# Kernel optimization log

Hardware: AMD Instinct MI355X
Metric: run time of the kernel (lower is better)

Reference implementation:

```python
import jax, jax.numpy as jnp
import numpy as np

B, D, K = 4, 128, 512   # batch, node_embedding_dim, num_nodes
ALPHA = 0.2             # LeakyReLU negative slope


def setup_inputs() -> dict:
    key = jax.random.key(0)
    k1, k2, k3, k4 = jax.random.split(key, 4)
    x = jax.random.normal(k1, (B, D, K), dtype=jnp.float32)
    # nn.Linear(2D -> D): store weight as (2D, D) for right-multiplication
    lin_w = jax.random.normal(k2, (2 * D, D), dtype=jnp.float32) * (1.0 / np.sqrt(2 * D))
    lin_b = jax.random.normal(k3, (D,), dtype=jnp.float32) * 0.01
    # attention vector a: (D,) (xavier-uniform in torch; scale-equivalent normal here)
    a = jax.random.normal(k4, (D,), dtype=jnp.float32) * (1.414 * np.sqrt(2.0 / (D + 1)))
    bias_mat = jnp.zeros((K, K), dtype=jnp.float32)  # init zeros per module
    return {"x": x, "lin_w": lin_w, "lin_b": lin_b, "a": a, "bias_mat": bias_mat}


def reference(x, lin_w, lin_b, a, bias_mat):
    # x: (B, D, K) -> transpose to (B, K, D); GATv2 path, residual = identity
    xt = jnp.swapaxes(x, 1, 2)                      # (B, K, D)
    d = xt.shape[-1]
    # lin(concat(v_i, v_j)) == v_i @ W1 + v_j @ W2 + b  (exact split; avoids (B,K,K,2D) concat)
    W1, W2 = lin_w[:d], lin_w[d:]
    left = xt @ W1 + lin_b                          # (B, K, D) -- v_i part (repeating block)
    right = xt @ W2                                 # (B, K, D) -- v_j part (alternating block)
    pre = left[:, :, None, :] + right[:, None, :, :]  # (B, K, K, D)
    h = jnp.where(pre > 0, pre, ALPHA * pre)        # LeakyReLU
    e = jnp.einsum('bijd,d->bij', h, a) + bias_mat  # (B, K, K)
    attn = jax.nn.softmax(e, axis=2)                # softmax over j (dropout p=0)
    agg = jnp.einsum('bij,bjd->bid', attn, xt)      # (B, K, D)
    out = jax.nn.sigmoid(agg) + xt                  # sigmoid + identity residual
    return jnp.swapaxes(out, 1, 2)                  # (B, D, K)
```

## Files before the change

### kernel.cpp

```cpp
#include <hip/hip_runtime.h>

#define B 4
#define D 128
#define K 512
#define TI 8

typedef __fp16 h2v __attribute__((ext_vector_type(2)));

__device__ __forceinline__ unsigned pkrtz(float a, float b) {
  h2v h = __builtin_amdgcn_cvt_pkrtz(a, b);
  union { h2v h; unsigned u; } c; c.h = h; return c.u;
}
__device__ __forceinline__ h2v u2h(unsigned u) {
  union { unsigned u; h2v h; } c; c.u = u; return c.h;
}
__device__ __forceinline__ float fdot2f(h2v a, h2v b, float c) {
#if __has_builtin(__builtin_amdgcn_fdot2)
  return __builtin_amdgcn_fdot2(a, b, c, false);
#else
  return c + (float)a.x * (float)b.x + (float)a.y * (float)b.y;
#endif
}
__device__ __forceinline__ h2v relu2(h2v a) {
#if __has_builtin(__builtin_elementwise_max)
  const h2v z = {(__fp16)0.f, (__fp16)0.f};
  return __builtin_elementwise_max(a, z);
#else
  h2v r;
  r.x = (float)a.x > 0.f ? a.x : (__fp16)0.f;
  r.y = (float)a.y > 0.f ? a.y : (__fp16)0.f;
  return r;
#endif
}

__global__ __launch_bounds__(256) void gat_lr16(
    const float* __restrict__ x, const float* __restrict__ lin_w,
    const float* __restrict__ lin_b, const float* __restrict__ a,
    unsigned* __restrict__ LhT, unsigned* __restrict__ RhT,
    unsigned* __restrict__ XhT) {
  const int j0 = blockIdx.x * 64;
  const int E0 = blockIdx.y * 16;
  const int b = blockIdx.z;
  const int t = threadIdx.x;
  __shared__ float sx[D][64];
  __shared__ float sw1[D][16];
  __shared__ float sw2[D][16];
#pragma unroll
  for (int r = 0; r < 8; ++r) {
    const int fid = t + 256 * r;
    const int row = fid >> 4, c4 = fid & 15;
    *(float4*)&sx[row][4 * c4] =
        *(const float4*)&x[((size_t)b * D + row) * K + j0 + 4 * c4];
  }
#pragma unroll
  for (int r = 0; r < 8; ++r) {
    const int idx = t + 256 * r;
    const int row = idx >> 4, e = idx & 15;
    sw1[row][e] = lin_w[(size_t)row * D + E0 + e];
    sw2[row][e] = lin_w[(size_t)(D + row) * D + E0 + e];
  }
  __syncthreads();
  {
    const int ry = blockIdx.y * 2;
#pragma unroll
    for (int r = ry; r < ry + 2; ++r) {
      const int idx = t + 256 * r;
      const int row = idx >> 5, jc = idx & 31;
      XhT[((size_t)b * D + row) * (K / 2) + (j0 >> 1) + jc] =
          pkrtz(sx[row][2 * jc], sx[row][2 * jc + 1]);
    }
  }
  const int j = t & 63, g = t >> 6;
  float accL[4] = {0.f, 0.f, 0.f, 0.f}, accR[4] = {0.f, 0.f, 0.f, 0.f};
#pragma unroll 8
  for (int c = 0; c < D; ++c) {
    const float xv = sx[c][j];
    const float4 w1 = *(const float4*)&sw1[c][4 * g];
    const float4 w2 = *(const float4*)&sw2[c][4 * g];
    accL[0] = fmaf(xv, w1.x, accL[0]);
    accL[1] = fmaf(xv, w1.y, accL[1]);
    accL[2] = fmaf(xv, w1.z, accL[2]);
    accL[3] = fmaf(xv, w1.w, accL[3]);
    accR[0] = fmaf(xv, w2.x, accR[0]);
    accR[1] = fmaf(xv, w2.y, accR[1]);
    accR[2] = fmaf(xv, w2.z, accR[2]);
    accR[3] = fmaf(xv, w2.w, accR[3]);
  }
  const int e0 = E0 + 4 * g;
#pragma unroll
  for (int u = 0; u < 2; ++u) {
    const int ea = e0 + 2 * u, eb = ea + 1;
    const float uea = 0.8f * fabsf(a[ea]), ueb = 0.8f * fabsf(a[eb]);
    const float La = uea * (accL[2 * u] + lin_b[ea]);
    const float Lb = ueb * (accL[2 * u + 1] + lin_b[eb]);
    const float Ra = uea * accR[2 * u];
    const float Rb = ueb * accR[2 * u + 1];
    const size_t dp = (size_t)(ea >> 1);
    LhT[((size_t)b * (D / 2) + dp) * K + j0 + j] = pkrtz(La, Lb);
    RhT[((size_t)b * (D / 2) + dp) * K + j0 + j] = pkrtz(Ra, Rb);
  }
}

__global__ __launch_bounds__(512, 2) void gat_attn16(
    const float* __restrict__ x, const float* __restrict__ a,
    const float* __restrict__ bias, const unsigned* __restrict__ LhT,
    const unsigned* __restrict__ RhT, const unsigned* __restrict__ XhT,
    float* __restrict__ out) {
  const int i0 = blockIdx.x * TI;
  const int b = blockIdx.y;
  const int t = threadIdx.x;
  __shared__ float sxt[D][TI];
  __shared__ unsigned slh[D / 2][TI];
  __shared__ unsigned ssg[D / 2];
  __shared__ float sSL[TI];
  __shared__ float seT[TI][K];
  __shared__ unsigned sattn16[TI][K / 2];

  {
    int idx = t;
    sxt[idx >> 3][idx & 7] = x[((size_t)b * D + (idx >> 3)) * K + i0 + (idx & 7)];
    idx = t + 512;
    sxt[idx >> 3][idx & 7] = x[((size_t)b * D + (idx >> 3)) * K + i0 + (idx & 7)];
    const int dp = t >> 3, ii = t & 7;
    slh[dp][ii] = LhT[((size_t)b * (D / 2) + dp) * K + i0 + ii];
    if (t < D / 2) {
      const float s0 = (a[2 * t] >= 0.f) ? 1.f : -1.f;
      const float s1 = (a[2 * t + 1] >= 0.f) ? 1.f : -1.f;
      ssg[t] = pkrtz(s0, s1);
    }
  }
  __syncthreads();
  {
    const int ii = t >> 6, dp = t & 63;
    float v = fdot2f(u2h(ssg[dp]), u2h(slh[dp][ii]), 0.f);
#pragma unroll
    for (int off = 32; off > 0; off >>= 1) v += __shfl_xor(v, off, 64);
    if ((t & 63) == 0) sSL[ii] = v;
  }
  __syncthreads();

  {
    const unsigned* rc = RhT + (size_t)b * (D / 2) * K + t;
    float acc[8] = {0.f, 0.f, 0.f, 0.f, 0.f, 0.f, 0.f, 0.f};
    float sr = 0.f;
#pragma unroll 8
    for (int dp = 0; dp < D / 2; ++dp) {
      const unsigned rr = rc[(size_t)dp * K];
      const uint4 lh4a = *(const uint4*)&slh[dp][0];
      const uint4 lh4b = *(const uint4*)&slh[dp][4];
      const h2v s2 = u2h(ssg[dp]);
      const h2v rv = u2h(rr);
      sr = fdot2f(s2, rv, sr);
      acc[0] = fdot2f(s2, relu2(u2h(lh4a.x) + rv), acc[0]);
      acc[1] = fdot2f(s2, relu2(u2h(lh4a.y) + rv), acc[1]);
      acc[2] = fdot2f(s2, relu2(u2h(lh4a.z) + rv), acc[2]);
      acc[3] = fdot2f(s2, relu2(u2h(lh4a.w) + rv), acc[3]);
      acc[4] = fdot2f(s2, relu2(u2h(lh4b.x) + rv), acc[4]);
      acc[5] = fdot2f(s2, relu2(u2h(lh4b.y) + rv), acc[5]);
      acc[6] = fdot2f(s2, relu2(u2h(lh4b.z) + rv), acc[6]);
      acc[7] = fdot2f(s2, relu2(u2h(lh4b.w) + rv), acc[7]);
    }
#pragma unroll
    for (int ii = 0; ii < TI; ++ii)
      seT[ii][t] = acc[ii] + 0.25f * (sSL[ii] + sr) +
                   bias[(size_t)(i0 + ii) * K + t];
  }
  __syncthreads();

  {
    const int w = t >> 6, lane = t & 63;
    float2 v[4];
    float m = -1e30f;
#pragma unroll
    for (int q = 0; q < 4; ++q) {
      v[q] = *(const float2*)&seT[w][2 * lane + 128 * q];
      m = fmaxf(m, fmaxf(v[q].x, v[q].y));
    }
#pragma unroll
    for (int off = 32; off > 0; off >>= 1) m = fmaxf(m, __shfl_xor(m, off, 64));
    float s = 0.f;
#pragma unroll
    for (int q = 0; q < 4; ++q) {
      v[q].x = __expf(v[q].x - m);
      v[q].y = __expf(v[q].y - m);
      s += v[q].x + v[q].y;
    }
#pragma unroll
    for (int off = 32; off > 0; off >>= 1) s += __shfl_xor(s, off, 64);
    const float inv = 1.f / s;
#pragma unroll
    for (int q = 0; q < 4; ++q)
      sattn16[w][lane + 64 * q] = pkrtz(v[q].x * inv, v[q].y * inv);
  }
  __syncthreads();

  {
    const int jr = t & 15, dg = t >> 4;
    uint4 ar[8][4];
#pragma unroll
    for (int i = 0; i < 8; ++i)
#pragma unroll
      for (int q = 0; q < 4; ++q)
        ar[i][q] = *(const uint4*)&sattn16[i][4 * (jr + 16 * q)];
    const unsigned* xh = XhT + (size_t)b * D * (K / 2);
#pragma unroll 2
    for (int r = 0; r < 4; ++r) {
      const int d = dg * 4 + r;
      float acc[8] = {0.f, 0.f, 0.f, 0.f, 0.f, 0.f, 0.f, 0.f};
#pragma unroll
      for (int q = 0; q < 4; ++q) {
        const uint4 xp =
            *(const uint4*)&xh[(size_t)d * (K / 2) + 4 * (jr + 16 * q)];
#pragma unroll
        for (int i = 0; i < 8; ++i) {
          acc[i] = fdot2f(u2h(ar[i][q].x), u2h(xp.x), acc[i]);
          acc[i] = fdot2f(u2h(ar[i][q].y), u2h(xp.y), acc[i]);
          acc[i] = fdot2f(u2h(ar[i][q].z), u2h(xp.z), acc[i]);
          acc[i] = fdot2f(u2h(ar[i][q].w), u2h(xp.w), acc[i]);
        }
      }
#pragma unroll
      for (int i = 0; i < 8; ++i) {
        acc[i] += __shfl_xor(acc[i], 1, 64);
        acc[i] += __shfl_xor(acc[i], 2, 64);
        acc[i] += __shfl_xor(acc[i], 4, 64);
        acc[i] += __shfl_xor(acc[i], 8, 64);
      }
      if (jr == 0) {
#pragma unroll
        for (int i = 0; i < 8; ++i) {
          const float sg = 1.f / (1.f + __expf(-acc[i]));
          out[((size_t)b * D + d) * K + i0 + i] = sg + sxt[d][i];
        }
      }
    }
  }
}

#define ALPHA 0.2f
__global__ __launch_bounds__(512) void gat_fused(
    const float* __restrict__ x, const float* __restrict__ lin_w,
    const float* __restrict__ lin_b, const float* __restrict__ a,
    const float* __restrict__ bias, float* __restrict__ out) {
  const int i = blockIdx.x, b = blockIdx.y, t = threadIdx.x;
  __shared__ float sxi[D], sLi[D], sa[D];
  __shared__ float lpart[4 * D];
  __shared__ float xtT[D * 64];
  __shared__ float epars[8 * 64];
  __shared__ float se[K];
  __shared__ float sattn[K], spart[K];
  __shared__ float sred[8];

  if (t < D) {
    sxi[t] = x[((size_t)b * D + t) * K + i];
    sa[t] = a[t];
  }
  __syncthreads();
  {
    const int c = t & (D - 1), q = t >> 7;
    float acc = 0.f;
    const float* W1 = lin_w + c;
#pragma unroll 8
    for (int d = q * 32; d < q * 32 + 32; ++d)
      acc = fmaf(sxi[d], W1[(size_t)d * D], acc);
    lpart[q * D + c] = acc;
  }
  __syncthreads();
  if (t < D)
    sLi[t] = lin_b[t] + lpart[t] + lpart[D + t] + lpart[2 * D + t] +
             lpart[3 * D + t];
  __syncthreads();

  for (int jt = 0; jt < K / 64; ++jt) {
    const int j0 = jt * 64;
    for (int idx = t; idx < D * 64; idx += 512)
      xtT[idx] = x[((size_t)b * D + (idx >> 6)) * K + j0 + (idx & 63)];
    __syncthreads();
    const int jj = t & 63, g = t >> 6, dp0 = g * 16;
    float accv[16];
#pragma unroll
    for (int v = 0; v < 16; ++v) accv[v] = 0.f;
    for (int dc = 0; dc < D; dc += 16) {
      float xv[16];
#pragma unroll
      for (int u = 0; u < 16; ++u) xv[u] = xtT[(dc + u) * 64 + jj];
#pragma unroll
      for (int u = 0; u < 16; ++u) {
        const float* W2r = lin_w + (size_t)(D + dc + u) * D + dp0;
#pragma unroll
        for (int v = 0; v < 16; ++v) accv[v] = fmaf(xv[u], W2r[v], accv[v]);
      }
    }
    float ep = 0.f;
#pragma unroll
    for (int v = 0; v < 16; ++v) {
      const float pre = sLi[dp0 + v] + accv[v];
      ep = fmaf(sa[dp0 + v], pre > 0.f ? pre : ALPHA * pre, ep);
    }
    epars[g * 64 + jj] = ep;
    __syncthreads();
    if (t < 64) {
      float esum = bias[(size_t)i * K + j0 + t];
#pragma unroll
      for (int g2 = 0; g2 < 8; ++g2) esum += epars[g2 * 64 + t];
      se[j0 + t] = esum;
    }
    __syncthreads();
  }

  float e = se[t];
  float m = e;
#pragma unroll
  for (int off = 32; off > 0; off >>= 1) m = fmaxf(m, __shfl_xor(m, off, 64));
  if ((t & 63) == 0) sred[t >> 6] = m;
  __syncthreads();
  m = sred[0];
#pragma unroll
  for (int w = 1; w < 8; ++w) m = fmaxf(m, sred[w]);
  const float ev = __expf(e - m);
  float s = ev;
#pragma unroll
  for (int off = 32; off > 0; off >>= 1) s += __shfl_xor(s, off, 64);
  __syncthreads();
  if ((t & 63) == 0) sred[t >> 6] = s;
  __syncthreads();
  s = 0.f;
#pragma unroll
  for (int w = 0; w < 8; ++w) s += sred[w];
  sattn[t] = ev * (1.f / s);
  __syncthreads();

  const int d = t >> 2, c = t & 3;
  const float4* X4 = (const float4*)(x + ((size_t)b * D + d) * K);
  const float4* A4 = (const float4*)sattn;
  float p = 0.f;
#pragma unroll 4
  for (int q = 0; q < K / 16; ++q) {
    const int idx = c + 4 * q;
    float4 xv = X4[idx], av = A4[idx];
    p = fmaf(av.x, xv.x, p);
    p = fmaf(av.y, xv.y, p);
    p = fmaf(av.z, xv.z, p);
    p = fmaf(av.w, xv.w, p);
  }
  spart[t] = p;
  __syncthreads();
  if (t < D) {
    const float agg =
        spart[4 * t] + spart[4 * t + 1] + spart[4 * t + 2] + spart[4 * t + 3];
    const float sg = 1.f / (1.f + __expf(-agg));
    out[((size_t)b * D + t) * K + i] = sg + sxi[t];
  }
}

extern "C" void kernel_launch(void* const* d_in, const int* in_sizes, int n_in,
                              void* d_out, int out_size, void* d_ws,
                              size_t ws_size, hipStream_t stream) {
  const float* x = (const float*)d_in[0];
  const float* lin_w = (const float*)d_in[1];
  const float* lin_b = (const float*)d_in[2];
  const float* a = (const float*)d_in[3];
  const float* bias = (const float*)d_in[4];
  float* out = (float*)d_out;

  const size_t half_words = (size_t)B * (D / 2) * K;
  const size_t xh_words = (size_t)B * D * (K / 2);
  const size_t need = (2 * half_words + xh_words) * sizeof(unsigned);
  if (ws_size >= need && d_ws != nullptr) {
    unsigned* LhT = (unsigned*)d_ws;
    unsigned* RhT = LhT + half_words;
    unsigned* XhT = RhT + half_words;
    gat_lr16<<<dim3(K / 64, D / 16, B), 256, 0, stream>>>(x, lin_w, lin_b, a,
                                                          LhT, RhT, XhT);
    gat_attn16<<<dim3(K / TI, B), 512, 0, stream>>>(x, a, bias, LhT, RhT, XhT,
                                                    out);
  } else {
    gat_fused<<<dim3(K, B), 512, 0, stream>>>(x, lin_w, lin_b, a, bias, out);
  }
}
```

Measured before the change: 85.12 us.

## Raise attn kernel occupancy by dropping LDS staging and restructuring aggregation registers

The attention kernel's launch bounds go from 2 to 4 blocks per CU. The shared-memory copies of x and the left projection are removed, and both are read straight from global memory (uint4 loads for LhT, float4 loads of x in the epilogue). The aggregation loop is restructured to keep 32 accumulators and load attention fragments in two halves, which lowers peak register pressure. The aim is more waves resident to hide latency, at the cost of more global or L2 traffic and possible spilling under the tighter register cap.

```diff
diff --git a/kernel.cpp b/kernel.cpp
--- a/kernel.cpp
+++ b/kernel.cpp
@@ -101,7 +101,7 @@
   }
 }
 
-__global__ __launch_bounds__(512, 2) void gat_attn16(
+__global__ __launch_bounds__(512, 4) void gat_attn16(
     const float* __restrict__ x, const float* __restrict__ a,
     const float* __restrict__ bias, const unsigned* __restrict__ LhT,
     const unsigned* __restrict__ RhT, const unsigned* __restrict__ XhT,
@@ -109,30 +109,21 @@
   const int i0 = blockIdx.x * TI;
   const int b = blockIdx.y;
   const int t = threadIdx.x;
-  __shared__ float sxt[D][TI];
-  __shared__ unsigned slh[D / 2][TI];
   __shared__ unsigned ssg[D / 2];
   __shared__ float sSL[TI];
   __shared__ float seT[TI][K];
   __shared__ unsigned sattn16[TI][K / 2];
 
-  {
-    int idx = t;
-    sxt[idx >> 3][idx & 7] = x[((size_t)b * D + (idx >> 3)) * K + i0 + (idx & 7)];
-    idx = t + 512;
-    sxt[idx >> 3][idx & 7] = x[((size_t)b * D + (idx >> 3)) * K + i0 + (idx & 7)];
-    const int dp = t >> 3, ii = t & 7;
-    slh[dp][ii] = LhT[((size_t)b * (D / 2) + dp) * K + i0 + ii];
-    if (t < D / 2) {
-      const float s0 = (a[2 * t] >= 0.f) ? 1.f : -1.f;
-      const float s1 = (a[2 * t + 1] >= 0.f) ? 1.f : -1.f;
-      ssg[t] = pkrtz(s0, s1);
-    }
+  if (t < D / 2) {
+    const float s0 = (a[2 * t] >= 0.f) ? 1.f : -1.f;
+    const float s1 = (a[2 * t + 1] >= 0.f) ? 1.f : -1.f;
+    ssg[t] = pkrtz(s0, s1);
   }
   __syncthreads();
   {
     const int ii = t >> 6, dp = t & 63;
-    float v = fdot2f(u2h(ssg[dp]), u2h(slh[dp][ii]), 0.f);
+    const unsigned lh = LhT[((size_t)b * (D / 2) + dp) * K + i0 + ii];
+    float v = fdot2f(u2h(ssg[dp]), u2h(lh), 0.f);
 #pragma unroll
     for (int off = 32; off > 0; off >>= 1) v += __shfl_xor(v, off, 64);
     if ((t & 63) == 0) sSL[ii] = v;
@@ -141,13 +132,14 @@
 
   {
     const unsigned* rc = RhT + (size_t)b * (D / 2) * K + t;
+    const unsigned* lrow = LhT + (size_t)b * (D / 2) * K + i0;
     float acc[8] = {0.f, 0.f, 0.f, 0.f, 0.f, 0.f, 0.f, 0.f};
     float sr = 0.f;
 #pragma unroll 8
     for (int dp = 0; dp < D / 2; ++dp) {
       const unsigned rr = rc[(size_t)dp * K];
-      const uint4 lh4a = *(const uint4*)&slh[dp][0];
-      const uint4 lh4b = *(const uint4*)&slh[dp][4];
+      const uint4 lh4a = *(const uint4*)&lrow[(size_t)dp * K];
+      const uint4 lh4b = *(const uint4*)&lrow[(size_t)dp * K + 4];
       const h2v s2 = u2h(ssg[dp]);
       const h2v rv = u2h(rr);
       sr = fdot2f(s2, rv, sr);
@@ -196,41 +188,59 @@
 
   {
     const int jr = t & 15, dg = t >> 4;
-    uint4 ar[8][4];
-#pragma unroll
-    for (int i = 0; i < 8; ++i)
-#pragma unroll
-      for (int q = 0; q < 4; ++q)
-        ar[i][q] = *(const uint4*)&sattn16[i][4 * (jr + 16 * q)];
     const unsigned* xh = XhT + (size_t)b * D * (K / 2);
-#pragma unroll 2
-    for (int r = 0; r < 4; ++r) {
-      const int d = dg * 4 + r;
-      float acc[8] = {0.f, 0.f, 0.f, 0.f, 0.f, 0.f, 0.f, 0.f};
-#pragma unroll
-      for (int q = 0; q < 4; ++q) {
-        const uint4 xp =
-            *(const uint4*)&xh[(size_t)d * (K / 2) + 4 * (jr + 16 * q)];
-#pragma unroll
-        for (int i = 0; i < 8; ++i) {
-          acc[i] = fdot2f(u2h(ar[i][q].x), u2h(xp.x), acc[i]);
-          acc[i] = fdot2f(u2h(ar[i][q].y), u2h(xp.y), acc[i]);
-          acc[i] = fdot2f(u2h(ar[i][q].z), u2h(xp.z), acc[i]);
-          acc[i] = fdot2f(u2h(ar[i][q].w), u2h(xp.w), acc[i]);
+    float accT[4][8];
+#pragma unroll
+    for (int r = 0; r < 4; ++r)
+#pragma unroll
+      for (int i = 0; i < 8; ++i) accT[r][i] = 0.f;
+#pragma unroll
+    for (int p = 0; p < 2; ++p) {
+      uint4 ar[8][2];
+#pragma unroll
+      for (int i = 0; i < 8; ++i)
+#pragma unroll
+        for (int qq = 0; qq < 2; ++qq)
+          ar[i][qq] = *(const uint4*)&sattn16[i][4 * (jr + 16 * (2 * p + qq))];
+#pragma unroll
+      for (int r = 0; r < 4; ++r) {
+        const int d = dg * 4 + r;
+#pragma unroll
+        for (int qq = 0; qq < 2; ++qq) {
+          const uint4 xp =
+              *(const uint4*)&xh[(size_t)d * (K / 2) +
+                                 4 * (jr + 16 * (2 * p + qq))];
+#pragma unroll
+          for (int i = 0; i < 8; ++i) {
+            accT[r][i] = fdot2f(u2h(ar[i][qq].x), u2h(xp.x), accT[r][i]);
+            accT[r][i] = fdot2f(u2h(ar[i][qq].y), u2h(xp.y), accT[r][i]);
+            accT[r][i] = fdot2f(u2h(ar[i][qq].z), u2h(xp.z), accT[r][i]);
+            accT[r][i] = fdot2f(u2h(ar[i][qq].w), u2h(xp.w), accT[r][i]);
+          }
         }
       }
+    }
+#pragma unroll
+    for (int r = 0; r < 4; ++r) {
 #pragma unroll
       for (int i = 0; i < 8; ++i) {
-        acc[i] += __shfl_xor(acc[i], 1, 64);
-        acc[i] += __shfl_xor(acc[i], 2, 64);
-        acc[i] += __shfl_xor(acc[i], 4, 64);
-        acc[i] += __shfl_xor(acc[i], 8, 64);
+        accT[r][i] += __shfl_xor(accT[r][i], 1, 64);
+        accT[r][i] += __shfl_xor(accT[r][i], 2, 64);
+        accT[r][i] += __shfl_xor(accT[r][i], 4, 64);
+        accT[r][i] += __shfl_xor(accT[r][i], 8, 64);
       }
       if (jr == 0) {
+        const int d = dg * 4 + r;
+        const float* xrow = x + ((size_t)b * D + d) * K + i0;
+        const float4 xv0 = *(const float4*)&xrow[0];
+        const float4 xv1 = *(const float4*)&xrow[4];
+        const float xr[8] = {xv0.x, xv0.y, xv0.z, xv0.w,
+                             xv1.x, xv1.y, xv1.z, xv1.w};
+        float* orow = out + ((size_t)b * D + d) * K + i0;
 #pragma unroll
         for (int i = 0; i < 8; ++i) {
-          const float sg = 1.f / (1.f + __expf(-acc[i]));
-          out[((size_t)b * D + d) * K + i0 + i] = sg + sxt[d][i];
+          const float sg = 1.f / (1.f + __expf(-accT[r][i]));
+          orow[i] = sg + xr[i];
         }
       }
     }
```

Result: slower. 108.2 us (+27.1%).
